# Kernel optimization log

Hardware: AMD Instinct MI355X
Metric: run time of the kernel (lower is better)

## Reference

```python
import jax, jax.numpy as jnp
import numpy as np

LMAX=4; MMAX=2; L2=25; M2=19; C=64; CE=64; NRBF=600; CUT=5.0
HEADS=8; ACH=32; VCH=16; HMSG=64; HFF=128; G=288; NL=2
AVG_NEI=20.0; AVG_NODES=2000.0
N_NODES=2000; N_EDGES=40000; NSPEC=90
# |m| group of each truncated (edge-frame) coefficient, order l=0..4, m=-min(l,2)..min(l,2)
MG = np.array([0, 1,0,1, 2,1,0,1,2, 2,1,0,1,2, 2,1,0,1,2])
# l of each full SH coefficient (25 total)
LOC = np.array([0] + [1]*3 + [2]*5 + [3]*7 + [4]*9)

def silu(x):
    return x * jax.nn.sigmoid(x)

def rms_norm_sh(x, w):
    # x: [N, 25, C]; w: [5, C] per-degree affine weight (rms_norm_sh)
    ms = jnp.mean(x * x, axis=1, keepdims=True)
    return x * jax.lax.rsqrt(ms + 1e-6) * w[LOC][None]

def setup_inputs() -> dict:
    key = jax.random.key(0)
    ks = iter(jax.random.split(key, 64))
    def rn(shape, scale):
        return jax.random.normal(next(ks), shape, dtype=jnp.float32) * scale
    inp = {}
    inp['edge_vectors'] = rn((N_EDGES, 3), 1.5)
    inp['wigner'] = rn((N_EDGES, M2, L2), 0.2)
    inp['wigner_inv'] = rn((N_EDGES, L2, M2), 0.2)
    inp['species_embed'] = rn((NSPEC, C), 1.0)
    inp['edge_species_embed'] = rn((NSPEC, 2 * CE), 1.0)
    DIN = NRBF + 2 * CE  # 728
    inp['deg_W1'] = rn((DIN, 128), DIN ** -0.5)
    inp['deg_b1'] = jnp.zeros((128,), jnp.float32)
    inp['deg_W2'] = rn((128, M2 * C), 128 ** -0.5)
    inp['deg_b2'] = jnp.zeros((M2 * C,), jnp.float32)
    inp['norm1_w'] = jnp.ones((NL, 5, C), jnp.float32)
    inp['rad_W1'] = rn((NL, DIN, 128), DIN ** -0.5)
    inp['rad_b1'] = jnp.zeros((NL, 128), jnp.float32)
    inp['rad_W2'] = rn((NL, 128, 3 * 2 * C), 128 ** -0.5)
    inp['rad_b2'] = jnp.ones((NL, 3 * 2 * C), jnp.float32)
    inp['so2_W'] = rn((NL, 3, 2 * C, HMSG), (2 * C) ** -0.5)
    inp['alpha_W'] = rn((NL, HMSG, HEADS * ACH), HMSG ** -0.5)
    inp['alpha_vec'] = rn((NL, HEADS, ACH), ACH ** -0.5)
    inp['value_W'] = rn((NL, 3, HMSG, HEADS * VCH), HMSG ** -0.5)
    inp['proj_W'] = rn((NL, 3, HEADS * VCH, C), (HEADS * VCH) ** -0.5)
    inp['norm2_w'] = jnp.ones((NL, 5, C), jnp.float32)
    inp['ffn_W1'] = rn((NL, C, HFF), C ** -0.5)
    inp['ffn_b1'] = jnp.zeros((NL, HFF), jnp.float32)
    inp['ffn_W2'] = rn((NL, HFF, C), HFF ** -0.5)
    inp['to_grid'] = rn((G, L2), L2 ** -0.5)
    inp['from_grid'] = rn((L2, G), G ** -0.5)
    inp['final_norm_w'] = jnp.ones((5, C), jnp.float32)
    inp['en_W1'] = rn((C, HFF), C ** -0.5)
    inp['en_b1'] = jnp.zeros((HFF,), jnp.float32)
    inp['en_W2'] = rn((HFF, 1), HFF ** -0.5)
    inp['en_b2'] = jnp.zeros((1,), jnp.float32)
    inp['node_species'] = jax.random.randint(next(ks), (N_NODES,), 0, NSPEC, dtype=jnp.int32)
    inp['senders'] = jax.random.randint(next(ks), (N_EDGES,), 0, N_NODES, dtype=jnp.int32)
    inp['receivers'] = jax.random.randint(next(ks), (N_EDGES,), 0, N_NODES, dtype=jnp.int32)
    inp['n_node'] = jnp.array([N_NODES], jnp.int32)
    return inp

def reference(edge_vectors, wigner, wigner_inv, species_embed, edge_species_embed,
              deg_W1, deg_b1, deg_W2, deg_b2, norm1_w, rad_W1, rad_b1, rad_W2, rad_b2,
              so2_W, alpha_W, alpha_vec, value_W, proj_W, norm2_w, ffn_W1, ffn_b1, ffn_W2,
              to_grid, from_grid, final_norm_w, en_W1, en_b1, en_W2, en_b2,
              node_species, senders, receivers, n_node):
    N = node_species.shape[0]
    E = senders.shape[0]
    mg = jnp.asarray(MG)
    # Gaussian RBF distance expansion (rbf_width=2.0)
    d = jnp.sqrt(jnp.sum(edge_vectors * edge_vectors, axis=-1) + 1e-12)
    offs = jnp.linspace(0.0, CUT, NRBF)
    std = 2.0 * (CUT / (NRBF - 1))
    rbf = jnp.exp(-0.5 * ((d[:, None] - offs[None, :]) / std) ** 2)  # [E, 600]
    # shared atom-edge embedding concat
    ne = edge_species_embed[node_species]
    se, re = jnp.split(ne, 2, axis=-1)
    ee = jnp.concatenate([rbf, se[senders], re[receivers]], axis=1)  # [E, 728]
    # initial node features: species embedding on l=0 component
    x = jnp.zeros((N, L2, C), dtype=edge_vectors.dtype).at[:, 0, :].set(species_embed[node_species])
    # edge degree embedding: radial MLP -> edge-frame coeffs -> rotate back -> scatter
    h = silu(ee @ deg_W1 + deg_b1) @ deg_W2 + deg_b2
    deg = jnp.einsum('elm,emc->elc', wigner_inv, h.reshape(E, M2, C))  # [E,25,C]
    x = x + jax.ops.segment_sum(deg, receivers, num_segments=N) / AVG_NEI
    for i in range(NL):
        # --- SO2 equivariant graph attention ---
        res = x
        xn = rms_norm_sh(x, norm1_w[i])
        msg = jnp.concatenate([xn[senders], xn[receivers]], axis=-1)      # [E,25,2C]
        msg = jnp.einsum('eml,elc->emc', wigner, msg)                     # rotate to edge frame [E,19,2C]
        rad = (silu(ee @ rad_W1[i] + rad_b1[i]) @ rad_W2[i] + rad_b2[i]).reshape(E, MMAX + 1, 2 * C)
        msg = msg * rad[:, mg]                                            # per-|m| radial modulation
        h = jnp.einsum('emc,mco->emo', msg, so2_W[i][mg])                 # SO2 conv [E,19,HMSG]
        a = (silu(h[:, 0, :]) @ alpha_W[i]).reshape(E, HEADS, ACH)        # invariant (m=0) alpha path
        logits = jnp.sum(silu(a) * alpha_vec[i][None], axis=-1)           # [E,HEADS]
        mx = jax.ops.segment_max(logits, receivers, num_segments=N)[receivers]
        ex = jnp.exp(logits - mx)
        den = jax.ops.segment_sum(ex, receivers, num_segments=N)[receivers]
        attn = ex / (den + 1e-12)
        v = jnp.einsum('emo,mov->emv', h, value_W[i][mg]).reshape(E, M2, HEADS, VCH)
        v = (v * attn[:, None, :, None]).reshape(E, M2, HEADS * VCH)
        oe = jnp.einsum('emv,mvc->emc', v, proj_W[i][mg])                 # [E,19,C]
        oe = jnp.einsum('elm,emc->elc', wigner_inv, oe)                   # rotate back [E,25,C]
        x = res + jax.ops.segment_sum(oe, receivers, num_segments=N)
        # --- S2 grid feed-forward ---
        res = x
        xn = rms_norm_sh(x, norm2_w[i])
        g = jnp.einsum('gl,nlc->ngc', to_grid, xn)                        # [N,288,C]
        g = silu(g @ ffn_W1[i] + ffn_b1[i]) @ ffn_W2[i]
        x = res + jnp.einsum('lg,ngc->nlc', from_grid, g)
    # final norm + energy head
    xn = rms_norm_sh(x, final_norm_w)
    g = jnp.einsum('gl,nlc->ngc', to_grid, xn)
    g = silu(g @ en_W1 + en_b1) @ en_W2 + en_b2
    eo = jnp.einsum('lg,ngo->nlo', from_grid, g)
    return eo[:, 0, 0] / AVG_NODES
```

## Files before the change

kernel.cpp:

```cpp
#include <hip/hip_runtime.h>
#include <hip/hip_bf16.h>
#include <math.h>


#define NRBF 600
#define DIN 728
#define GPTS 288
#define CH 8

typedef __attribute__((ext_vector_type(8))) short bf16x8;
typedef __attribute__((ext_vector_type(4))) float f32x4;

__constant__ int d_mg[19] = {0,1,0,1,2,1,0,1,2,2,1,0,1,2,2,1,0,1,2};
__constant__ int d_loc[25] = {0,1,1,1,2,2,2,2,2,3,3,3,3,3,3,3,4,4,4,4,4,4,4,4,4};
__constant__ int d_mg0[5]={0,2,6,11,16};
__constant__ int d_mg1[8]={1,3,5,7,10,12,15,17};
__constant__ int d_mg2[6]={4,8,9,13,14,18};

__device__ inline float silu_f(float v){ return v/(1.0f+__expf(-v)); }
__device__ inline float bf2f(unsigned short u){ return __uint_as_float(((unsigned)u)<<16); }
__device__ inline unsigned short f2bf(float f){
  unsigned b=__float_as_uint(f);
  return (unsigned short)((b + 0x7FFF + ((b>>16)&1)) >> 16);
}

__device__ inline void atomicMaxF(float* addr, float val){
  int* ia=(int*)addr;
  int old=*ia;
  while (__int_as_float(old) < val){
    int assumed=old;
    old = atomicCAS(ia, assumed, __float_as_int(val));
    if (old == assumed) break;
  }
}

__global__ __launch_bounds__(256) void zero_cnt_kernel(int* cnt, int N){
  int i = blockIdx.x*256+threadIdx.x;
  if (i<N) cnt[i]=0;
}
__global__ __launch_bounds__(256) void csr_count_kernel(const int* __restrict__ rcv, int* cnt, int E){
  int i = blockIdx.x*256+threadIdx.x;
  if (i<E) atomicAdd(&cnt[rcv[i]],1);
}
__global__ __launch_bounds__(256) void csr_scan_kernel(const int* __restrict__ cnt,
    int* rowptr, int* fill, int N){
  __shared__ int s_part[256];
  int tid=threadIdx.x;
  int chunk=(N+255)/256;
  int lvals[12];
  int base=tid*chunk;
  int lsum=0;
  for (int i=0;i<chunk && i<12;i++){
    int v=(base+i<N)?cnt[base+i]:0;
    lvals[i]=lsum; lsum+=v;
  }
  s_part[tid]=lsum;
  __syncthreads();
  if (tid==0){
    int run=0;
    for (int t=0;t<256;t++){ int v=s_part[t]; s_part[t]=run; run+=v; }
  }
  __syncthreads();
  int off=s_part[tid];
  for (int i=0;i<chunk && i<12;i++){
    if (base+i<N){ rowptr[base+i]=off+lvals[i]; fill[base+i]=off+lvals[i]; }
  }
  if (tid==255) rowptr[N]=off+lsum;
}
__global__ __launch_bounds__(256) void csr_fill_kernel(const int* __restrict__ rcv,
    int* fill, int* eix, int E){
  int i = blockIdx.x*256+threadIdx.x;
  if (i<E){ int p=atomicAdd(&fill[rcv[i]],1); eix[p]=i; }
}

__global__ __launch_bounds__(256) void wsvb_kernel(const float* __restrict__ so2W,
    const float* __restrict__ valW, unsigned short* __restrict__ wsvb){
  int i=blockIdx.x/3, g=blockIdx.x%3;
  const float* A = so2W + (size_t)i*24576 + g*8192;
  const float* B = valW + (size_t)i*24576 + g*8192;
  unsigned short* C = wsvb + (size_t)blockIdx.x*16384;
  __shared__ float sB[8192];
  for (int j=threadIdx.x;j<2048;j+=256) ((float4*)sB)[j]=((const float4*)B)[j];
  __syncthreads();
  for (int idx=threadIdx.x; idx<16384; idx+=256){
    int k=idx>>7, j=idx&127;
    float acc=0;
    #pragma unroll 4
    for (int o=0;o<64;o++) acc += A[k*64+o]*sB[o*128+j];
    int pos = ((k>>5)*8 + (j>>4))*512 + (((k>>3)&3)*16 + (j&15))*8 + (k&7);
    C[pos]=f2bf(acc);
  }
}

__global__ __launch_bounds__(256) void projb_kernel(const float* __restrict__ pW,
    unsigned short* __restrict__ projb){
  const float* src = pW + (size_t)blockIdx.x*8192;
  unsigned short* dst = projb + (size_t)blockIdx.x*8192;
  for (int idx=threadIdx.x; idx<8192; idx+=256){
    int k=idx>>6, j=idx&63;
    int pos = ((k>>5)*4 + (j>>4))*512 + (((k>>3)&3)*16 + (j&15))*8 + (k&7);
    dst[pos]=f2bf(src[idx]);
  }
}

__global__ __launch_bounds__(256) void packB2g_kernel(const float* __restrict__ src,
    unsigned short* __restrict__ dh, unsigned short* __restrict__ dl, int K, int Nn){
  int ktiles=(K+31)>>5;
  int nnt=Nn>>4;
  int tot=ktiles*nnt*512;
  for (int idx=blockIdx.x*256+threadIdx.x; idx<tot; idx+=gridDim.x*256){
    int f=idx>>9, r=idx&511, lane=r>>3, j=r&7;
    int kt=f/nnt, nt=f-kt*nnt;
    int k=kt*32+(lane>>4)*8+j, c=nt*16+(lane&15);
    float v=(k<K)? src[k*Nn+c] : 0.0f;
    unsigned short h=f2bf(v);
    dh[idx]=h;
    dl[idx]=f2bf(v-bf2f(h));
  }
}

__global__ __launch_bounds__(256) void pack_tg2_kernel(const float* __restrict__ tg,
    unsigned short* __restrict__ tgp){
  int tid=threadIdx.x;
  for (int idx=tid; idx<9216; idx+=256){
    int t=idx>>9, r=idx&511, lane=r>>3, j=r&7;
    int kl=(lane>>4)*8+j, row=t*16+(lane&15);
    float v=(kl<25)? tg[row*25+kl] : 0.0f;
    unsigned short h=f2bf(v);
    tgp[idx]=h;
    tgp[9216+idx]=f2bf(v-bf2f(h));
  }
}

__global__ __launch_bounds__(256) void pack_fg2_kernel(const float* __restrict__ fg,
    unsigned short* __restrict__ fgp){
  int tid=threadIdx.x;
  for (int idx=tid; idx<18432; idx+=256){
    int f=idx>>9, r=idx&511, lane=r>>3, j=r&7;
    int t=f>>1, mt=f&1;
    int row=mt*16+(lane&15), k=(lane>>4)*8+j;
    float v=(row<25 && k<16)? fg[row*288+t*16+k] : 0.0f;
    unsigned short h=f2bf(v);
    fgp[idx]=h;
    fgp[18432+idx]=f2bf(v-bf2f(h));
  }
}

__global__ __launch_bounds__(256) void mlpf_kernel(const float* __restrict__ ev,
    const float* __restrict__ ese, const int* __restrict__ nsp,
    const unsigned short* __restrict__ dw1h, const unsigned short* __restrict__ dw1l,
    const float* __restrict__ db1,
    const unsigned short* __restrict__ dw2h, const unsigned short* __restrict__ dw2l,
    const float* __restrict__ db2,
    const unsigned short* __restrict__ r1h, const unsigned short* __restrict__ r1l,
    const float* __restrict__ rb1,
    const unsigned short* __restrict__ r2h, const unsigned short* __restrict__ r2l,
    const float* __restrict__ rb2,
    const int* __restrict__ snd, const int* __restrict__ rcv, const int* __restrict__ eix,
    int do_deg,
    unsigned short* __restrict__ degout, float* __restrict__ radout, int E){
  int tid=threadIdx.x, wv=tid>>6, lane=tid&63;
  int lanelo=lane&15, khi=lane>>4;
  int p0=blockIdx.x*16;
  __shared__ unsigned short s_eeh[4096], s_eel[4096];
  __shared__ unsigned short s_h1h[2048], s_h1l[2048];
  __shared__ float s_d[16]; __shared__ int s_ss[16], s_rs[16], s_e[16];
  if (tid<16){
    int p=p0+tid;
    int e=(p<E)? eix[p] : -1;
    s_e[tid]=e;
    if (e>=0){
      float vx=ev[3*e], vy=ev[3*e+1], vz=ev[3*e+2];
      s_d[tid]=sqrtf(vx*vx+vy*vy+vz*vz+1e-12f);
      s_ss[tid]=nsp[snd[e]]; s_rs[tid]=nsp[rcv[e]];
    } else { s_d[tid]=0.0f; s_ss[tid]=0; s_rs[tid]=0; }
  }
  __syncthreads();
  const float step=5.0f/599.0f, inv_std=1.0f/(2.0f*step);
  int nta=wv*2, ntb=nta+1;
  f32x4 z4={0,0,0,0};
  f32x4 aD0=z4,aD1=z4,aR0=z4,aR1=z4;
  for (int c=0;c<23;c+=CH){
    int ncur=23-c; if (ncur>CH) ncur=CH;
    for (int idx=tid; idx<ncur*512; idx+=256){
      int f=idx>>9, r=idx&511, ln=r>>3, j=r&7;
      int k=(c+f)*32+((ln>>4)<<3)+j, row=ln&15;
      float v=0.0f;
      if (k<NRBF){ float t=(s_d[row]-k*step)*inv_std; v=__expf(-0.5f*t*t); }
      else if (k<NRBF+64) v=ese[s_ss[row]*128+(k-NRBF)];
      else if (k<DIN)     v=ese[s_rs[row]*128+64+(k-NRBF-64)];
      unsigned short h=f2bf(v);
      s_eeh[idx]=h; s_eel[idx]=f2bf(v-bf2f(h));
    }
    __syncthreads();
    for (int f=0; f<ncur; f++){
      int kt=c+f;
      bf16x8 Ah=*(const bf16x8*)(s_eeh + f*512 + lane*8);
      bf16x8 Al=*(const bf16x8*)(s_eel + f*512 + lane*8);
      size_t ba=(size_t)(kt*8+nta)*512+lane*8;
      {
        bf16x8 Bh=*(const bf16x8*)(r1h+ba), Bl=*(const bf16x8*)(r1l+ba);
        bf16x8 Bh2=*(const bf16x8*)(r1h+ba+512), Bl2=*(const bf16x8*)(r1l+ba+512);
        aR0=__builtin_amdgcn_mfma_f32_16x16x32_bf16(Ah,Bh,aR0,0,0,0);
        aR0=__builtin_amdgcn_mfma_f32_16x16x32_bf16(Al,Bh,aR0,0,0,0);
        aR0=__builtin_amdgcn_mfma_f32_16x16x32_bf16(Ah,Bl,aR0,0,0,0);
        aR1=__builtin_amdgcn_mfma_f32_16x16x32_bf16(Ah,Bh2,aR1,0,0,0);
        aR1=__builtin_amdgcn_mfma_f32_16x16x32_bf16(Al,Bh2,aR1,0,0,0);
        aR1=__builtin_amdgcn_mfma_f32_16x16x32_bf16(Ah,Bl2,aR1,0,0,0);
      }
      if (do_deg){
        bf16x8 Bh=*(const bf16x8*)(dw1h+ba), Bl=*(const bf16x8*)(dw1l+ba);
        bf16x8 Bh2=*(const bf16x8*)(dw1h+ba+512), Bl2=*(const bf16x8*)(dw1l+ba+512);
        aD0=__builtin_amdgcn_mfma_f32_16x16x32_bf16(Ah,Bh,aD0,0,0,0);
        aD0=__builtin_amdgcn_mfma_f32_16x16x32_bf16(Al,Bh,aD0,0,0,0);
        aD0=__builtin_amdgcn_mfma_f32_16x16x32_bf16(Ah,Bl,aD0,0,0,0);
        aD1=__builtin_amdgcn_mfma_f32_16x16x32_bf16(Ah,Bh2,aD1,0,0,0);
        aD1=__builtin_amdgcn_mfma_f32_16x16x32_bf16(Al,Bh2,aD1,0,0,0);
        aD1=__builtin_amdgcn_mfma_f32_16x16x32_bf16(Ah,Bl2,aD1,0,0,0);
      }
    }
    __syncthreads();
  }
  int nmlp = do_deg ? 2 : 1;
  #pragma unroll 1
  for (int it=0; it<nmlp; it++){
    int is_deg = (it==1);
    f32x4 a0 = is_deg ? aD0 : aR0;
    f32x4 a1 = is_deg ? aD1 : aR1;
    const float* b1 = is_deg ? db1 : rb1;
    #pragma unroll
    for (int q=0;q<4;q++){
      int row=khi*4+q;
      {
        int col=nta*16+lanelo;
        float v=silu_f(a0[q]+b1[col]);
        int pos=row*128 + (((col>>3)^(row&7))<<3) + (col&7);
        unsigned short h=f2bf(v);
        s_h1h[pos]=h; s_h1l[pos]=f2bf(v-bf2f(h));
      }
      {
        int col=ntb*16+lanelo;
        float v=silu_f(a1[q]+b1[col]);
        int pos=row*128 + (((col>>3)^(row&7))<<3) + (col&7);
        unsigned short h=f2bf(v);
        s_h1h[pos]=h; s_h1l[pos]=f2bf(v-bf2f(h));
      }
    }
    __syncthreads();
    bf16x8 Ahh[4],Ahl[4];
    #pragma unroll
    for (int kt=0;kt<4;kt++){
      int o=lanelo*128 + (((kt*4+khi)^(lanelo&7))<<3);
      Ahh[kt]=*(const bf16x8*)(s_h1h+o);
      Ahl[kt]=*(const bf16x8*)(s_h1l+o);
    }
    __syncthreads();
    if (is_deg){
      for (int nt=wv; nt<76; nt+=4){
        f32x4 acc=z4;
        #pragma unroll
        for (int kt=0;kt<4;kt++){
          size_t bo=(size_t)(kt*76+nt)*512+lane*8;
          bf16x8 Bh=*(const bf16x8*)(dw2h+bo), Bl=*(const bf16x8*)(dw2l+bo);
          acc=__builtin_amdgcn_mfma_f32_16x16x32_bf16(Ahh[kt],Bh,acc,0,0,0);
          acc=__builtin_amdgcn_mfma_f32_16x16x32_bf16(Ahl[kt],Bh,acc,0,0,0);
          acc=__builtin_amdgcn_mfma_f32_16x16x32_bf16(Ahh[kt],Bl,acc,0,0,0);
        }
        int col=nt*16+lanelo;
        float bb=db2[col];
        #pragma unroll
        for (int q=0;q<4;q++){
          int p=p0+khi*4+q;
          if (p<E) degout[(size_t)p*1216+col]=f2bf(acc[q]+bb);
        }
      }
    } else {
      for (int nt=wv; nt<24; nt+=4){
        f32x4 acc=z4;
        #pragma unroll
        for (int kt=0;kt<4;kt++){
          size_t bo=(size_t)(kt*24+nt)*512+lane*8;
          bf16x8 Bh=*(const bf16x8*)(r2h+bo), Bl=*(const bf16x8*)(r2l+bo);
          acc=__builtin_amdgcn_mfma_f32_16x16x32_bf16(Ahh[kt],Bh,acc,0,0,0);
          acc=__builtin_amdgcn_mfma_f32_16x16x32_bf16(Ahl[kt],Bh,acc,0,0,0);
          acc=__builtin_amdgcn_mfma_f32_16x16x32_bf16(Ahh[kt],Bl,acc,0,0,0);
        }
        int col=nt*16+lanelo;
        float bb=rb2[col];
        #pragma unroll
        for (int q=0;q<4;q++){
          int e=s_e[khi*4+q];
          if (e>=0) radout[(size_t)e*384+col]=acc[q]+bb;
        }
      }
    }
  }
}

__global__ __launch_bounds__(256) void node_sum_kernel(const unsigned short* __restrict__ msgb,
    const float* __restrict__ winv, const int* __restrict__ rowptr, const int* __restrict__ eix,
    const int* __restrict__ nsp, const float* __restrict__ spe,
    const float* __restrict__ nw, float* __restrict__ x, float* __restrict__ xn,
    int mode, int N){
  int n=blockIdx.x, tid=threadIdx.x, wv=tid>>6, lane=tid&63;
  __shared__ float s_winv[4][480];
  __shared__ unsigned short s_oe[4][1216];
  __shared__ float4 s_red[4][400];
  __shared__ float4 s_ms4[16];
  int row0=rowptr[n];
  int cnt=rowptr[n+1]-row0;
  float4 acc[7];
  #pragma unroll
  for (int t=0;t<7;t++) acc[t]=make_float4(0,0,0,0);
  for (int j=wv; j<cnt; j+=4){
    int p=row0+j;
    int e=eix[p];
    asm volatile("s_waitcnt lgkmcnt(0)" ::: "memory");
    for (int k=lane;k<475;k+=64) s_winv[wv][k]=winv[(size_t)e*475+k];
    if (mode==1){
      for (int k=lane;k<152;k+=64)
        ((int4*)s_oe[wv])[k]=*(const int4*)(msgb+(size_t)p*1216+k*8);
    } else {
      for (int k=lane;k<152;k+=64){
        int m=k>>3, jj=k&7;
        ((int4*)s_oe[wv])[k]=*(const int4*)(msgb+(size_t)p*2432+m*128+jj*8);
      }
    }
    asm volatile("s_waitcnt lgkmcnt(0)" ::: "memory");
    const unsigned* o2=(const unsigned*)s_oe[wv];
    #pragma unroll
    for (int t=0;t<7;t++){
      int sI=lane+t*64;
      if (sI<400){
        int l=sI>>4, c4=sI&15;
        const float* wr=s_winv[wv]+l*19;
        float4 a=acc[t];
        #pragma unroll
        for (int m=0;m<19;m++){
          float w=wr[m];
          unsigned ua=o2[m*32+c4*2], ub=o2[m*32+c4*2+1];
          a.x+=w*bf2f((unsigned short)(ua&0xffffu));
          a.y+=w*bf2f((unsigned short)(ua>>16));
          a.z+=w*bf2f((unsigned short)(ub&0xffffu));
          a.w+=w*bf2f((unsigned short)(ub>>16));
        }
        acc[t]=a;
      }
    }
  }
  asm volatile("s_waitcnt lgkmcnt(0)" ::: "memory");
  #pragma unroll
  for (int t=0;t<7;t++){
    int sI=lane+t*64;
    if (sI<400) s_red[wv][sI]=acc[t];
  }
  __syncthreads();
  float4* xp=(float4*)(x+(size_t)n*1600);
  int j0=tid, j1=tid+256;
  bool h1=(j1<400);
  float4 v0, v1=make_float4(0,0,0,0);
  if (mode==0){
    {
      float4 a=s_red[0][j0], b=s_red[1][j0], c=s_red[2][j0], d=s_red[3][j0];
      float4 cur=xp[j0];
      cur.x+=a.x+b.x+c.x+d.x;
      cur.y+=a.y+b.y+c.y+d.y;
      cur.z+=a.z+b.z+c.z+d.z;
      cur.w+=a.w+b.w+c.w+d.w;
      v0=cur; xp[j0]=cur;
    }
    if (h1){
      float4 a=s_red[0][j1], b=s_red[1][j1], c=s_red[2][j1], d=s_red[3][j1];
      float4 cur=xp[j1];
      cur.x+=a.x+b.x+c.x+d.x;
      cur.y+=a.y+b.y+c.y+d.y;
      cur.z+=a.z+b.z+c.z+d.z;
      cur.w+=a.w+b.w+c.w+d.w;
      v1=cur; xp[j1]=cur;
    }
  } else {
    int sp=nsp[n];
    const float4* sp4=(const float4*)(spe+(size_t)sp*64);
    {
      int l=j0>>4, c4=j0&15;
      float4 a=s_red[0][j0], b=s_red[1][j0], c=s_red[2][j0], d=s_red[3][j0];
      float4 base=(l==0)? sp4[c4] : make_float4(0,0,0,0);
      float4 o;
      o.x=base.x+0.05f*(a.x+b.x+c.x+d.x);
      o.y=base.y+0.05f*(a.y+b.y+c.y+d.y);
      o.z=base.z+0.05f*(a.z+b.z+c.z+d.z);
      o.w=base.w+0.05f*(a.w+b.w+c.w+d.w);
      v0=o; xp[j0]=o;
    }
    if (h1){
      float4 a=s_red[0][j1], b=s_red[1][j1], c=s_red[2][j1], d=s_red[3][j1];
      float4 o;
      o.x=0.05f*(a.x+b.x+c.x+d.x);
      o.y=0.05f*(a.y+b.y+c.y+d.y);
      o.z=0.05f*(a.z+b.z+c.z+d.z);
      o.w=0.05f*(a.w+b.w+c.w+d.w);
      v1=o; xp[j1]=o;
    }
  }
  __syncthreads();
  float4* s_p4=(float4*)s_red;
  float4 a4;
  a4.x=v0.x*v0.x; a4.y=v0.y*v0.y; a4.z=v0.z*v0.z; a4.w=v0.w*v0.w;
  if (h1){ a4.x+=v1.x*v1.x; a4.y+=v1.y*v1.y; a4.z+=v1.z*v1.z; a4.w+=v1.w*v1.w; }
  s_p4[tid]=a4;
  __syncthreads();
  if (tid<16){
    float4 s=make_float4(0,0,0,0);
    #pragma unroll
    for (int k=0;k<16;k++){
      float4 p=s_p4[tid+16*k];
      s.x+=p.x; s.y+=p.y; s.z+=p.z; s.w+=p.w;
    }
    float4 m;
    m.x=rsqrtf(s.x*(1.0f/25.0f)+1e-6f);
    m.y=rsqrtf(s.y*(1.0f/25.0f)+1e-6f);
    m.z=rsqrtf(s.z*(1.0f/25.0f)+1e-6f);
    m.w=rsqrtf(s.w*(1.0f/25.0f)+1e-6f);
    s_ms4[tid]=m;
  }
  __syncthreads();
  float4* xnp=(float4*)(xn+(size_t)n*1600);
  {
    int l=j0>>4, g=j0&15;
    float4 m=s_ms4[g];
    const float* wr=nw + d_loc[l]*64 + g*4;
    float4 o;
    o.x=v0.x*m.x*wr[0]; o.y=v0.y*m.y*wr[1]; o.z=v0.z*m.z*wr[2]; o.w=v0.w*m.w*wr[3];
    xnp[j0]=o;
  }
  if (h1){
    int l=j1>>4, g=j1&15;
    float4 m=s_ms4[g];
    const float* wr=nw + d_loc[l]*64 + g*4;
    float4 o;
    o.x=v1.x*m.x*wr[0]; o.y=v1.y*m.y*wr[1]; o.z=v1.z*m.z*wr[2]; o.w=v1.w*m.w*wr[3];
    xnp[j1]=o;
  }
}

__global__ __launch_bounds__(256) void init_mxden_kernel(float* mx, float* den, int N){
  int idx = blockIdx.x*256+threadIdx.x;
  if (idx < N*8){ mx[idx]=-3.0e38f; den[idx]=0.0f; }
}

__global__ __launch_bounds__(256) void den_kernel(const float* __restrict__ logits,
    const float* __restrict__ mx, const int* __restrict__ rcv,
    float* __restrict__ den, int E){
  int idx = blockIdx.x*256+threadIdx.x;
  if (idx >= E*8) return;
  int e = idx>>3, hd = idx&7, r = rcv[e];
  atomicAdd(&den[r*8+hd], __expf(logits[idx]-mx[r*8+hd]));
}

__global__ __launch_bounds__(256) void msg_kernel(const float* __restrict__ xn,
    const float* __restrict__ wig, const float* __restrict__ radb,
    const float* __restrict__ so2W, const float* __restrict__ alphaW, const float* __restrict__ alphaV,
    const int* __restrict__ snd, const int* __restrict__ rcv, const int* __restrict__ eix,
    unsigned short* __restrict__ msgb, float* __restrict__ logits, float* __restrict__ mx, int E){
  __shared__ float s_wig[1900];
  __shared__ float s_m0[4][128];
  __shared__ float s_sh0[4][64];
  int tid=threadIdx.x, wv=tid>>6, lane=tid&63;
  int p=blockIdx.x*4+wv;
  bool act=(p<E);
  int pc=act? p : (E-1);
  int e=eix[pc];
  int node=(lane<32)? snd[e] : rcv[e];
  int c2=(lane&31)*2;
  int col0=c2+((lane>>5)<<6);
  const float* xb=xn+(size_t)node*1600+c2;
  float ca[25], cb[25];
  #pragma unroll
  for (int l=0;l<25;l++){
    float2 v=*(const float2*)(xb+l*64);
    ca[l]=v.x; cb[l]=v.y;
  }
  float* swig=s_wig+wv*475;
  for (int j=lane;j<475;j+=64) swig[j]=wig[(size_t)e*475+j];
  float ra0,ra1,rb0,rb1,rc0,rc1;
  {
    const float* rb_=radb+(size_t)e*384;
    float2 v0=*(const float2*)(rb_+col0);
    float2 v1=*(const float2*)(rb_+128+col0);
    float2 v2=*(const float2*)(rb_+256+col0);
    ra0=v0.x; ra1=v0.y; rb0=v1.x; rb1=v1.y; rc0=v2.x; rc1=v2.y;
  }
  __syncthreads();
  unsigned short* dst=msgb+(size_t)pc*2432+col0;
  constexpr int mgc[19]={0,1,0,1,2,1,0,1,2,2,1,0,1,2,2,1,0,1,2};
  float m0a=0.0f, m0b=0.0f;
  if (act){
    #pragma unroll
    for (int m=0;m<19;m++){
      float a0=0.0f,a1=0.0f;
      const float* wr=swig+m*25;
      #pragma unroll
      for (int l=0;l<25;l++){ float w=wr[l]; a0+=w*ca[l]; a1+=w*cb[l]; }
      float r0,r1;
      if (mgc[m]==0){ r0=ra0; r1=ra1; }
      else if (mgc[m]==1){ r0=rb0; r1=rb1; }
      else { r0=rc0; r1=rc1; }
      a0*=r0; a1*=r1;
      if (m==0){ m0a=a0; m0b=a1; }
      unsigned packv=((unsigned)f2bf(a1)<<16)|(unsigned)f2bf(a0);
      *(unsigned*)(dst+m*128)=packv;
    }
  }
  s_m0[wv][col0]=m0a; s_m0[wv][col0+1]=m0b;
  asm volatile("s_waitcnt lgkmcnt(0)" ::: "memory");
  {
    const float* m0p=s_m0[wv];
    float accs=0.0f;
    #pragma unroll 8
    for (int k=0;k<128;k++) accs += m0p[k]*so2W[k*64+lane];
    s_sh0[wv][lane]=silu_f(accs);
  }
  asm volatile("s_waitcnt lgkmcnt(0)" ::: "memory");
  {
    const float* sh=s_sh0[wv];
    int j0=lane*4;
    float4 av=*(const float4*)(alphaV+j0);
    float4 aacc={0,0,0,0};
    #pragma unroll 8
    for (int o=0;o<64;o++){
      float s=sh[o];
      float4 w=*(const float4*)(alphaW+o*256+j0);
      aacc.x+=s*w.x; aacc.y+=s*w.y; aacc.z+=s*w.z; aacc.w+=s*w.w;
    }
    float part = silu_f(aacc.x)*av.x + silu_f(aacc.y)*av.y
               + silu_f(aacc.z)*av.z + silu_f(aacc.w)*av.w;
    part += __shfl_xor(part,1);
    part += __shfl_xor(part,2);
    part += __shfl_xor(part,4);
    if (act && (lane&7)==0){
      int h=lane>>3;
      int r=rcv[e];
      logits[(size_t)e*8+h]=part;
      atomicMaxF(&mx[r*8+h], part);
    }
  }
}

__global__ __launch_bounds__(256) void attn_gemm_kernel(unsigned short* __restrict__ msgb,
    const unsigned short* __restrict__ wsvp, const unsigned short* __restrict__ projp,
    const float* __restrict__ logits, const float* __restrict__ mx, const float* __restrict__ den,
    const int* __restrict__ eix, const int* __restrict__ rcv, int E){
  int tid=threadIdx.x, wv=tid>>6, lane=tid&63;
  int lanelo=lane&15, khi=lane>>4;
  int p0=blockIdx.x*16;
  __shared__ unsigned short s_vv[2176];
  __shared__ float s_attn[16][8];
  __shared__ short s_r2e[304], s_r2m[304];
  for (int j=tid;j<304;j+=256){
    int e,m;
    if (j<80){ e=j/5; m=d_mg0[j%5]; }
    else if (j<208){ int q=j-80; e=q>>3; m=d_mg1[q&7]; }
    else { int q=j-208; e=q/6; m=d_mg2[q%6]; }
    s_r2e[j]=(short)e; s_r2m[j]=(short)m;
  }
  if (tid<128){
    int i=tid>>3, h=tid&7, p=p0+i;
    float a=0.0f;
    if (p<E){
      int e=eix[p]; int r=rcv[e];
      a=__expf(logits[(size_t)e*8+h]-mx[r*8+h])/(den[r*8+h]+1e-12f);
    }
    s_attn[i][h]=a;
  }
  __syncthreads();
  const int4* wp4=(const int4*)wsvp;
  const int4* pp4=(const int4*)projp;
  for (int t=0;t<19;t++){
    int g=(t<5)?0:((t<13)?1:2);
    int R=t*16+lanelo;
    int ei=s_r2e[R], mi=s_r2m[R];
    int pp=p0+ei;
    size_t abase=((size_t)((pp<E)?pp:0))*2432 + (size_t)mi*128;
    bf16x8 A[4];
    #pragma unroll
    for (int kt=0;kt<4;kt++)
      A[kt]=*(const bf16x8*)(msgb + abase + kt*32 + khi*8);
    #pragma unroll
    for (int h2=0;h2<2;h2++){
      int nt=wv*2+h2;
      f32x4 acc={0,0,0,0};
      #pragma unroll
      for (int kt=0;kt<4;kt++){
        int4 tt=wp4[g*2048+(kt*8+nt)*64+lane];
        acc=__builtin_amdgcn_mfma_f32_16x16x32_bf16(A[kt],*(bf16x8*)&tt,acc,0,0,0);
      }
      int col=nt*16+lanelo;
      #pragma unroll
      for (int q=0;q<4;q++){
        int r16=khi*4+q;
        int ei2=s_r2e[t*16+r16];
        s_vv[r16*136+col]=f2bf(acc[q]*s_attn[ei2][nt]);
      }
    }
    __syncthreads();
    {
      bf16x8 A2[4];
      #pragma unroll
      for (int kt=0;kt<4;kt++)
        A2[kt]=*(const bf16x8*)(s_vv + lanelo*136 + kt*32 + khi*8);
      f32x4 acc={0,0,0,0};
      #pragma unroll
      for (int kt=0;kt<4;kt++){
        int4 tt=pp4[g*1024+(kt*4+wv)*64+lane];
        acc=__builtin_amdgcn_mfma_f32_16x16x32_bf16(A2[kt],*(bf16x8*)&tt,acc,0,0,0);
      }
      int col=wv*16+lanelo;
      #pragma unroll
      for (int q=0;q<4;q++){
        int R2=t*16+khi*4+q;
        int pi=p0+s_r2e[R2];
        if (pi<E) msgb[(size_t)pi*2432 + (size_t)s_r2m[R2]*128 + col]=f2bf(acc[q]);
      }
    }
    __syncthreads();
  }
}

__global__ __launch_bounds__(256) void grid_ffn_mfma_kernel(const float* __restrict__ xnin,
    const unsigned short* __restrict__ tgp, const unsigned short* __restrict__ fgp,
    const unsigned short* __restrict__ w1p, const unsigned short* __restrict__ w2p,
    const float* __restrict__ b1, const float* __restrict__ nw,
    float* __restrict__ x, float* __restrict__ xnout, int N){
  int n=blockIdx.x, tid=threadIdx.x, wv=tid>>6, lane=tid&63;
  int lanelo=lane&15, khi=lane>>4;
  __shared__ __align__(16) char s_mem[74240];
  unsigned short* s_w1=(unsigned short*)s_mem;
  unsigned short* s_xn=(unsigned short*)(s_mem+32768);
  float* s_b1=(float*)(s_mem+40960);
  unsigned short* scr=(unsigned short*)(s_mem+41472)+(size_t)wv*4096;
  for (int j=tid;j<2048;j+=256) ((int4*)s_w1)[j]=((const int4*)w1p)[j];
  if (tid<128) s_b1[tid]=b1[tid];
  { int4 z={0,0,0,0}; for (int j=tid;j<512;j+=256) ((int4*)s_xn)[j]=z; }
  __syncthreads();
  {
    const float* xr=xnin+(size_t)n*1600;
    for (int j=tid;j<1600;j+=256){
      int k=j>>6, c=j&63;
      float v=xr[j];
      unsigned short h=f2bf(v);
      s_xn[c*32+k]=h;
      s_xn[2048+c*32+k]=f2bf(v-bf2f(h));
    }
  }
  __syncthreads();
  bf16x8 XBh[4],XBl[4];
  #pragma unroll
  for (int ct=0;ct<4;ct++){
    int o=(ct*16+lanelo)*32 + khi*8;
    XBh[ct]=*(const bf16x8*)(s_xn+o);
    XBl[ct]=*(const bf16x8*)(s_xn+2048+o);
  }
  f32x4 oacc[2][4];
  #pragma unroll
  for (int mt=0;mt<2;mt++)
    #pragma unroll
    for (int nt=0;nt<4;nt++){ f32x4 z={0,0,0,0}; oacc[mt][nt]=z; }
  for (int t=wv;t<18;t+=4){
    bf16x8 Atgh=*(const bf16x8*)(tgp + t*512 + lane*8);
    bf16x8 Atgl=*(const bf16x8*)(tgp + 9216 + t*512 + lane*8);
    #pragma unroll
    for (int ct=0;ct<4;ct++){
      f32x4 g={0,0,0,0};
      g=__builtin_amdgcn_mfma_f32_16x16x32_bf16(Atgh,XBh[ct],g,0,0,0);
      g=__builtin_amdgcn_mfma_f32_16x16x32_bf16(Atgl,XBh[ct],g,0,0,0);
      g=__builtin_amdgcn_mfma_f32_16x16x32_bf16(Atgh,XBl[ct],g,0,0,0);
      #pragma unroll
      for (int q=0;q<4;q++){
        int row=khi*4+q, col=ct*16+lanelo;
        int pos=row*64 + (((col>>3)^(row&7))<<3) + (col&7);
        float v=g[q]; unsigned short h=f2bf(v);
        scr[pos]=h; scr[1024+pos]=f2bf(v-bf2f(h));
      }
    }
    bf16x8 Agh[2],Agl[2];
    #pragma unroll
    for (int kt=0;kt<2;kt++){
      int o=lanelo*64 + (((kt*4+khi)^(lanelo&7))<<3);
      Agh[kt]=*(const bf16x8*)(scr+o);
      Agl[kt]=*(const bf16x8*)(scr+1024+o);
    }
    #pragma unroll
    for (int nt=0;nt<8;nt++){
      f32x4 h={0,0,0,0};
      #pragma unroll
      for (int kt=0;kt<2;kt++){
        bf16x8 Bh=*(const bf16x8*)(s_w1 + (kt*8+nt)*512 + lane*8);
        bf16x8 Bl=*(const bf16x8*)(s_w1 + 8192 + (kt*8+nt)*512 + lane*8);
        h=__builtin_amdgcn_mfma_f32_16x16x32_bf16(Agh[kt],Bh,h,0,0,0);
        h=__builtin_amdgcn_mfma_f32_16x16x32_bf16(Agl[kt],Bh,h,0,0,0);
        h=__builtin_amdgcn_mfma_f32_16x16x32_bf16(Agh[kt],Bl,h,0,0,0);
      }
      #pragma unroll
      for (int q=0;q<4;q++){
        int row=khi*4+q, col=nt*16+lanelo;
        float v=silu_f(h[q]+s_b1[col]);
        int pos=row*128 + (((col>>3)^(row&7))<<3) + (col&7);
        unsigned short hh=f2bf(v);
        scr[pos]=hh; scr[2048+pos]=f2bf(v-bf2f(hh));
      }
    }
    bf16x8 Ahh[4],Ahl[4];
    #pragma unroll
    for (int kt=0;kt<4;kt++){
      int o=lanelo*128 + (((kt*4+khi)^(lanelo&7))<<3);
      Ahh[kt]=*(const bf16x8*)(scr+o);
      Ahl[kt]=*(const bf16x8*)(scr+2048+o);
    }
    #pragma unroll
    for (int nt=0;nt<4;nt++){
      f32x4 o4={0,0,0,0};
      #pragma unroll
      for (int kt=0;kt<4;kt++){
        bf16x8 Bh=*(const bf16x8*)(w2p + (kt*4+nt)*512 + lane*8);
        bf16x8 Bl=*(const bf16x8*)(w2p + 8192 + (kt*4+nt)*512 + lane*8);
        o4=__builtin_amdgcn_mfma_f32_16x16x32_bf16(Ahh[kt],Bh,o4,0,0,0);
        o4=__builtin_amdgcn_mfma_f32_16x16x32_bf16(Ahl[kt],Bh,o4,0,0,0);
        o4=__builtin_amdgcn_mfma_f32_16x16x32_bf16(Ahh[kt],Bl,o4,0,0,0);
      }
      #pragma unroll
      for (int q=0;q<4;q++){
        int ch=nt*16+lanelo, rowk=khi*4+q;
        int pos=ch*32 + (((rowk>>3)^(ch&3))<<3) + (rowk&7);
        float v=o4[q]; unsigned short hh=f2bf(v);
        scr[pos]=hh; scr[2048+pos]=f2bf(v-bf2f(hh));
      }
    }
    bf16x8 Boh[4],Bol[4];
    #pragma unroll
    for (int nt=0;nt<4;nt++){
      int ch=nt*16+lanelo;
      int o=ch*32 + ((khi^(ch&3))<<3);
      Boh[nt]=*(const bf16x8*)(scr+o);
      Bol[nt]=*(const bf16x8*)(scr+2048+o);
    }
    #pragma unroll
    for (int mt=0;mt<2;mt++){
      bf16x8 Afh=*(const bf16x8*)(fgp + (t*2+mt)*512 + lane*8);
      bf16x8 Afl=*(const bf16x8*)(fgp + 18432 + (t*2+mt)*512 + lane*8);
      #pragma unroll
      for (int nt=0;nt<4;nt++){
        oacc[mt][nt]=__builtin_amdgcn_mfma_f32_16x16x32_bf16(Afh,Boh[nt],oacc[mt][nt],0,0,0);
        oacc[mt][nt]=__builtin_amdgcn_mfma_f32_16x16x32_bf16(Afl,Boh[nt],oacc[mt][nt],0,0,0);
        oacc[mt][nt]=__builtin_amdgcn_mfma_f32_16x16x32_bf16(Afh,Bol[nt],oacc[mt][nt],0,0,0);
      }
    }
  }
  __syncthreads();
  float* pout=(float*)s_mem;
  #pragma unroll
  for (int mt=0;mt<2;mt++)
    #pragma unroll
    for (int nt=0;nt<4;nt++)
      #pragma unroll
      for (int q=0;q<4;q++){
        int row=mt*16+khi*4+q, col=nt*16+lanelo;
        pout[wv*2048 + row*64 + col]=oacc[mt][nt][q];
      }
  __syncthreads();
  const size_t nb=(size_t)n*1600;
  float accn=0.0f;
  for (int j=tid;j<1600;j+=256){
    float v = x[nb+j] + pout[j]+pout[2048+j]+pout[4096+j]+pout[6144+j];
    x[nb+j]=v;
    accn += v*v;
  }
  __syncthreads();
  float* s_part=(float*)s_mem;
  float* s_msv=((float*)s_mem)+256;
  s_part[tid]=accn;
  __syncthreads();
  if (tid<64){
    float m=(s_part[tid]+s_part[tid+64]+s_part[tid+128]+s_part[tid+192])*(1.0f/25.0f);
    s_msv[tid]=rsqrtf(m+1e-6f);
  }
  __syncthreads();
  for (int j=tid;j<1600;j+=256){
    int l=j>>6, c=j&63;
    xnout[nb+j]=x[nb+j]*s_msv[c]*nw[d_loc[l]*64+c];
  }
}

__global__ __launch_bounds__(256) void energy_mfma_kernel(const float* __restrict__ xn,
    const unsigned short* __restrict__ tgp, const float* __restrict__ fg,
    const unsigned short* __restrict__ enw1p, const float* __restrict__ b1,
    const float* __restrict__ w2, const float* __restrict__ b2,
    float* __restrict__ out, int N){
  int n=blockIdx.x, tid=threadIdx.x, wv=tid>>6, lane=tid&63;
  int lanelo=lane&15, khi=lane>>4;
  __shared__ __align__(16) char s_mem[59584];
  unsigned short* s_w1=(unsigned short*)s_mem;
  unsigned short* s_xn=(unsigned short*)(s_mem+32768);
  float* s_b1=(float*)(s_mem+40960);
  float* s_w2=(float*)(s_mem+41472);
  float* s_fg0=(float*)(s_mem+41984);
  float* s_red=(float*)(s_mem+43136);
  unsigned short* scr=(unsigned short*)(s_mem+43200)+(size_t)wv*2048;
  for (int j=tid;j<2048;j+=256) ((int4*)s_w1)[j]=((const int4*)enw1p)[j];
  if (tid<128){ s_b1[tid]=b1[tid]; s_w2[tid]=w2[tid]; }
  for (int j=tid;j<288;j+=256) s_fg0[j]=fg[j];
  { int4 z={0,0,0,0}; for (int j=tid;j<512;j+=256) ((int4*)s_xn)[j]=z; }
  __syncthreads();
  {
    const float* xr=xn+(size_t)n*1600;
    for (int j=tid;j<1600;j+=256){
      int k=j>>6, c=j&63;
      float v=xr[j];
      unsigned short h=f2bf(v);
      s_xn[c*32+k]=h;
      s_xn[2048+c*32+k]=f2bf(v-bf2f(h));
    }
  }
  __syncthreads();
  bf16x8 XBh[4],XBl[4];
  #pragma unroll
  for (int ct=0;ct<4;ct++){
    int o=(ct*16+lanelo)*32 + khi*8;
    XBh[ct]=*(const bf16x8*)(s_xn+o);
    XBl[ct]=*(const bf16x8*)(s_xn+2048+o);
  }
  float b2v=b2[0];
  float e=0.0f;
  for (int t=wv;t<18;t+=4){
    bf16x8 Atgh=*(const bf16x8*)(tgp + t*512 + lane*8);
    bf16x8 Atgl=*(const bf16x8*)(tgp + 9216 + t*512 + lane*8);
    #pragma unroll
    for (int ct=0;ct<4;ct++){
      f32x4 g={0,0,0,0};
      g=__builtin_amdgcn_mfma_f32_16x16x32_bf16(Atgh,XBh[ct],g,0,0,0);
      g=__builtin_amdgcn_mfma_f32_16x16x32_bf16(Atgl,XBh[ct],g,0,0,0);
      g=__builtin_amdgcn_mfma_f32_16x16x32_bf16(Atgh,XBl[ct],g,0,0,0);
      #pragma unroll
      for (int q=0;q<4;q++){
        int row=khi*4+q, col=ct*16+lanelo;
        int pos=row*64 + (((col>>3)^(row&7))<<3) + (col&7);
        float v=g[q]; unsigned short h=f2bf(v);
        scr[pos]=h; scr[1024+pos]=f2bf(v-bf2f(h));
      }
    }
    bf16x8 Agh[2],Agl[2];
    #pragma unroll
    for (int kt=0;kt<2;kt++){
      int o=lanelo*64 + (((kt*4+khi)^(lanelo&7))<<3);
      Agh[kt]=*(const bf16x8*)(scr+o);
      Agl[kt]=*(const bf16x8*)(scr+1024+o);
    }
    #pragma unroll
    for (int nt=0;nt<8;nt++){
      f32x4 h={0,0,0,0};
      #pragma unroll
      for (int kt=0;kt<2;kt++){
        bf16x8 Bh=*(const bf16x8*)(s_w1 + (kt*8+nt)*512 + lane*8);
        bf16x8 Bl=*(const bf16x8*)(s_w1 + 8192 + (kt*8+nt)*512 + lane*8);
        h=__builtin_amdgcn_mfma_f32_16x16x32_bf16(Agh[kt],Bh,h,0,0,0);
        h=__builtin_amdgcn_mfma_f32_16x16x32_bf16(Agl[kt],Bh,h,0,0,0);
        h=__builtin_amdgcn_mfma_f32_16x16x32_bf16(Agh[kt],Bl,h,0,0,0);
      }
      #pragma unroll
      for (int q=0;q<4;q++){
        int row=khi*4+q, col=nt*16+lanelo;
        float v=silu_f(h[q]+s_b1[col]);
        e += v*s_w2[col]*s_fg0[t*16+row];
      }
    }
    if (lanelo==0){
      #pragma unroll
      for (int q=0;q<4;q++) e += s_fg0[t*16+khi*4+q]*b2v;
    }
  }
  #pragma unroll
  for (int d=1;d<64;d<<=1) e += __shfl_xor(e,d);
  if (lane==0) s_red[wv]=e;
  __syncthreads();
  if (tid==0) out[n]=(s_red[0]+s_red[1]+s_red[2]+s_red[3])*(1.0f/2000.0f);
}

extern "C" void kernel_launch(void* const* d_in, const int* in_sizes, int n_in,
                              void* d_out, int out_size, void* d_ws, size_t ws_size,
                              hipStream_t stream){
  (void)n_in; (void)out_size; (void)ws_size;
  const float* ev   = (const float*)d_in[0];
  const float* wig  = (const float*)d_in[1];
  const float* winv = (const float*)d_in[2];
  const float* spe  = (const float*)d_in[3];
  const float* ese  = (const float*)d_in[4];
  const float* degW1= (const float*)d_in[5];
  const float* degb1= (const float*)d_in[6];
  const float* degW2= (const float*)d_in[7];
  const float* degb2= (const float*)d_in[8];
  const float* n1w  = (const float*)d_in[9];
  const float* radW1= (const float*)d_in[10];
  const float* radb1= (const float*)d_in[11];
  const float* radW2= (const float*)d_in[12];
  const float* radb2= (const float*)d_in[13];
  const float* so2W = (const float*)d_in[14];
  const float* aW   = (const float*)d_in[15];
  const float* aV   = (const float*)d_in[16];
  const float* vW   = (const float*)d_in[17];
  const float* pW   = (const float*)d_in[18];
  const float* n2w  = (const float*)d_in[19];
  const float* fW1  = (const float*)d_in[20];
  const float* fb1  = (const float*)d_in[21];
  const float* fW2  = (const float*)d_in[22];
  const float* tg   = (const float*)d_in[23];
  const float* fg   = (const float*)d_in[24];
  const float* fnw  = (const float*)d_in[25];
  const float* enW1 = (const float*)d_in[26];
  const float* enb1 = (const float*)d_in[27];
  const float* enW2 = (const float*)d_in[28];
  const float* enb2 = (const float*)d_in[29];
  const int* nsp = (const int*)d_in[30];
  const int* snd = (const int*)d_in[31];
  const int* rcv = (const int*)d_in[32];
  int N = in_sizes[30];
  int E = in_sizes[31];
  float* out = (float*)d_out;

  float* ws = (float*)d_ws;
  size_t off = 0;
  float* radbuf = ws + off; off += (size_t)E*384;
  float* logits = ws + off; off += (size_t)E*8;
  float* mx     = ws + off; off += (size_t)N*8;
  float* den    = ws + off; off += (size_t)N*8;
  float* x      = ws + off; off += (size_t)N*1600;
  float* xn     = ws + off; off += (size_t)N*1600;
  unsigned short* wsvb  = (unsigned short*)(ws + off); off += (size_t)6*16384/2;
  unsigned short* projb = (unsigned short*)(ws + off); off += (size_t)6*8192/2;
  int* cnt      = (int*)(ws + off); off += (size_t)N;
  int* rowptr   = (int*)(ws + off); off += (size_t)(N+1);
  int* fill     = (int*)(ws + off); off += (size_t)N;
  int* eixbuf   = (int*)(ws + off); off += (size_t)E;
  off = (off + 3) & ~((size_t)3);
  unsigned short* msgb  = (unsigned short*)(ws + off); off += (size_t)E*1216;
  unsigned short* tgp   = (unsigned short*)(ws + off); off += 9216;
  unsigned short* fgp   = (unsigned short*)(ws + off); off += 18432;
  unsigned short* wwp   = (unsigned short*)(ws + off); off += 32768;
  unsigned short* enw1p = (unsigned short*)(ws + off); off += 8192;
  unsigned short* degw1p = (unsigned short*)(ws + off); off += 94208;
  unsigned short* degw2p = (unsigned short*)(ws + off); off += 155648;
  unsigned short* radw1p = (unsigned short*)(ws + off); off += 94208*2;
  unsigned short* radw2p = (unsigned short*)(ws + off); off += 49152*2;

  zero_cnt_kernel<<<(N+255)/256, 256, 0, stream>>>(cnt, N);
  csr_count_kernel<<<(E+255)/256, 256, 0, stream>>>(rcv, cnt, E);
  csr_scan_kernel<<<1, 256, 0, stream>>>(cnt, rowptr, fill, N);
  csr_fill_kernel<<<(E+255)/256, 256, 0, stream>>>(rcv, fill, eixbuf, E);
  wsvb_kernel<<<6, 256, 0, stream>>>(so2W, vW, wsvb);
  projb_kernel<<<6, 256, 0, stream>>>(pW, projb);
  pack_tg2_kernel<<<1, 256, 0, stream>>>(tg, tgp);
  pack_fg2_kernel<<<1, 256, 0, stream>>>(fg, fgp);
  for (int i=0;i<2;i++){
    unsigned short* wl = wwp + (size_t)i*32768;
    packB2g_kernel<<<8, 256, 0, stream>>>(fW1 + (size_t)i*8192, wl, wl+8192, 64, 128);
    packB2g_kernel<<<8, 256, 0, stream>>>(fW2 + (size_t)i*8192, wl+16384, wl+24576, 128, 64);
  }
  packB2g_kernel<<<8, 256, 0, stream>>>(enW1, enw1p, enw1p+8192, 64, 128);
  packB2g_kernel<<<32, 256, 0, stream>>>(degW1, degw1p, degw1p+94208, DIN, 128);
  packB2g_kernel<<<32, 256, 0, stream>>>(degW2, degw2p, degw2p+155648, 128, 1216);
  for (int i=0;i<2;i++){
    unsigned short* r1 = radw1p + (size_t)i*188416;
    unsigned short* r2 = radw2p + (size_t)i*98304;
    packB2g_kernel<<<32, 256, 0, stream>>>(radW1 + (size_t)i*DIN*128, r1, r1+94208, DIN, 128);
    packB2g_kernel<<<16, 256, 0, stream>>>(radW2 + (size_t)i*128*384, r2, r2+49152, 128, 384);
  }

  mlpf_kernel<<<(E+15)/16, 256, 0, stream>>>(ev, ese, nsp,
      degw1p, degw1p+94208, degb1, degw2p, degw2p+155648, degb2,
      radw1p, radw1p+94208, radb1,
      radw2p, radw2p+49152, radb2,
      snd, rcv, eixbuf, 1, msgb, radbuf, E);
  node_sum_kernel<<<N, 256, 0, stream>>>(msgb, winv, rowptr, eixbuf, nsp, spe,
                                         n1w, x, xn, 1, N);

  for (int i=0;i<2;i++){
    if (i==1){
      unsigned short* r1 = radw1p + (size_t)188416;
      unsigned short* r2 = radw2p + (size_t)98304;
      mlpf_kernel<<<(E+15)/16, 256, 0, stream>>>(ev, ese, nsp,
          degw1p, degw1p+94208, degb1, degw2p, degw2p+155648, degb2,
          r1, r1+94208, radb1+128,
          r2, r2+49152, radb2+384,
          snd, rcv, eixbuf, 0, msgb, radbuf, E);
    }
    init_mxden_kernel<<<(N*8+255)/256, 256, 0, stream>>>(mx, den, N);
    msg_kernel<<<(E+3)/4, 256, 0, stream>>>(xn, wig, radbuf,
                                            so2W + (size_t)i*24576,
                                            aW + (size_t)i*64*256, aV + (size_t)i*256,
                                            snd, rcv, eixbuf, msgb, logits, mx, E);
    den_kernel<<<(E*8+255)/256, 256, 0, stream>>>(logits, mx, rcv, den, E);
    attn_gemm_kernel<<<(E+15)/16, 256, 0, stream>>>(msgb,
                                                    wsvb + (size_t)i*3*16384, projb + (size_t)i*3*8192,
                                                    logits, mx, den, eixbuf, rcv, E);
    node_sum_kernel<<<N, 256, 0, stream>>>(msgb, winv, rowptr, eixbuf, nsp, spe,
                                           n2w + (size_t)i*320, x, xn, 0, N);
    const float* nxt = (i==0) ? (n1w + 320) : fnw;
    grid_ffn_mfma_kernel<<<N, 256, 0, stream>>>(xn, tgp, fgp,
                                                wwp + (size_t)i*32768, wwp + (size_t)i*32768 + 16384,
                                                fb1 + (size_t)i*128, nxt, x, xn, N);
  }
  energy_mfma_kernel<<<N, 256, 0, stream>>>(xn, tgp, fg, enw1p, enb1, enW2, enb2, out, N);
}
```

Measured before the change: 2.731 ms.

## Fuse both layers' radial MLPs into the single edge-feature MLP kernel

The second mlpf launch for layer 1 is removed. The first launch now computes the radial MLP hidden layers for both layers, alongside the degree MLP, from the same RBF and species feature tiles, so those features are built once. Radial outputs are stored as bf16 in two separate buffers instead of fp32, which halves the radial write and read traffic in msg_kernel. The cost is higher register pressure in the fused kernel and lower precision for the radial weights.

Result: slower. 2.806 ms (+2.8%).

```diff
diff --git a/kernel.cpp b/kernel.cpp
--- a/kernel.cpp
+++ b/kernel.cpp
@@ -152,13 +152,17 @@
     const float* __restrict__ db1,
     const unsigned short* __restrict__ dw2h, const unsigned short* __restrict__ dw2l,
     const float* __restrict__ db2,
-    const unsigned short* __restrict__ r1h, const unsigned short* __restrict__ r1l,
-    const float* __restrict__ rb1,
-    const unsigned short* __restrict__ r2h, const unsigned short* __restrict__ r2l,
-    const float* __restrict__ rb2,
+    const unsigned short* __restrict__ r1h0, const unsigned short* __restrict__ r1l0,
+    const float* __restrict__ rb10,
+    const unsigned short* __restrict__ r2h0, const unsigned short* __restrict__ r2l0,
+    const float* __restrict__ rb20,
+    const unsigned short* __restrict__ r1h1, const unsigned short* __restrict__ r1l1,
+    const float* __restrict__ rb11,
+    const unsigned short* __restrict__ r2h1, const unsigned short* __restrict__ r2l1,
+    const float* __restrict__ rb21,
     const int* __restrict__ snd, const int* __restrict__ rcv, const int* __restrict__ eix,
-    int do_deg,
-    unsigned short* __restrict__ degout, float* __restrict__ radout, int E){
+    unsigned short* __restrict__ degout,
+    unsigned short* __restrict__ rad0out, unsigned short* __restrict__ rad1out, int E){
   int tid=threadIdx.x, wv=tid>>6, lane=tid&63;
   int lanelo=lane&15, khi=lane>>4;
   int p0=blockIdx.x*16;
@@ -179,7 +183,7 @@
   const float step=5.0f/599.0f, inv_std=1.0f/(2.0f*step);
   int nta=wv*2, ntb=nta+1;
   f32x4 z4={0,0,0,0};
-  f32x4 aD0=z4,aD1=z4,aR0=z4,aR1=z4;
+  f32x4 aD0=z4,aD1=z4,aR0=z4,aR1=z4,aS0=z4,aS1=z4;
   for (int c=0;c<23;c+=CH){
     int ncur=23-c; if (ncur>CH) ncur=CH;
     for (int idx=tid; idx<ncur*512; idx+=256){
@@ -199,8 +203,8 @@
       bf16x8 Al=*(const bf16x8*)(s_eel + f*512 + lane*8);
       size_t ba=(size_t)(kt*8+nta)*512+lane*8;
       {
-        bf16x8 Bh=*(const bf16x8*)(r1h+ba), Bl=*(const bf16x8*)(r1l+ba);
-        bf16x8 Bh2=*(const bf16x8*)(r1h+ba+512), Bl2=*(const bf16x8*)(r1l+ba+512);
+        bf16x8 Bh=*(const bf16x8*)(r1h0+ba), Bl=*(const bf16x8*)(r1l0+ba);
+        bf16x8 Bh2=*(const bf16x8*)(r1h0+ba+512), Bl2=*(const bf16x8*)(r1l0+ba+512);
         aR0=__builtin_amdgcn_mfma_f32_16x16x32_bf16(Ah,Bh,aR0,0,0,0);
         aR0=__builtin_amdgcn_mfma_f32_16x16x32_bf16(Al,Bh,aR0,0,0,0);
         aR0=__builtin_amdgcn_mfma_f32_16x16x32_bf16(Ah,Bl,aR0,0,0,0);
@@ -208,7 +212,17 @@
         aR1=__builtin_amdgcn_mfma_f32_16x16x32_bf16(Al,Bh2,aR1,0,0,0);
         aR1=__builtin_amdgcn_mfma_f32_16x16x32_bf16(Ah,Bl2,aR1,0,0,0);
       }
-      if (do_deg){
+      {
+        bf16x8 Bh=*(const bf16x8*)(r1h1+ba), Bl=*(const bf16x8*)(r1l1+ba);
+        bf16x8 Bh2=*(const bf16x8*)(r1h1+ba+512), Bl2=*(const bf16x8*)(r1l1+ba+512);
+        aS0=__builtin_amdgcn_mfma_f32_16x16x32_bf16(Ah,Bh,aS0,0,0,0);
+        aS0=__builtin_amdgcn_mfma_f32_16x16x32_bf16(Al,Bh,aS0,0,0,0);
+        aS0=__builtin_amdgcn_mfma_f32_16x16x32_bf16(Ah,Bl,aS0,0,0,0);
+        aS1=__builtin_amdgcn_mfma_f32_16x16x32_bf16(Ah,Bh2,aS1,0,0,0);
+        aS1=__builtin_amdgcn_mfma_f32_16x16x32_bf16(Al,Bh2,aS1,0,0,0);
+        aS1=__builtin_amdgcn_mfma_f32_16x16x32_bf16(Ah,Bl2,aS1,0,0,0);
+      }
+      {
         bf16x8 Bh=*(const bf16x8*)(dw1h+ba), Bl=*(const bf16x8*)(dw1l+ba);
         bf16x8 Bh2=*(const bf16x8*)(dw1h+ba+512), Bl2=*(const bf16x8*)(dw1l+ba+512);
         aD0=__builtin_amdgcn_mfma_f32_16x16x32_bf16(Ah,Bh,aD0,0,0,0);
@@ -221,13 +235,11 @@
     }
     __syncthreads();
   }
-  int nmlp = do_deg ? 2 : 1;
   #pragma unroll 1
-  for (int it=0; it<nmlp; it++){
-    int is_deg = (it==1);
-    f32x4 a0 = is_deg ? aD0 : aR0;
-    f32x4 a1 = is_deg ? aD1 : aR1;
-    const float* b1 = is_deg ? db1 : rb1;
+  for (int it=0; it<3; it++){
+    f32x4 a0 = (it==0)? aR0 : (it==1)? aS0 : aD0;
+    f32x4 a1 = (it==0)? aR1 : (it==1)? aS1 : aD1;
+    const float* b1 = (it==0)? rb10 : (it==1)? rb11 : db1;
     #pragma unroll
     for (int q=0;q<4;q++){
       int row=khi*4+q;
@@ -255,7 +267,7 @@
       Ahl[kt]=*(const bf16x8*)(s_h1l+o);
     }
     __syncthreads();
-    if (is_deg){
+    if (it==2){
       for (int nt=wv; nt<76; nt+=4){
         f32x4 acc=z4;
         #pragma unroll
@@ -275,22 +287,26 @@
         }
       }
     } else {
+      const unsigned short* w2h = (it==0)? r2h0 : r2h1;
+      const unsigned short* w2l = (it==0)? r2l0 : r2l1;
+      const float* b2p = (it==0)? rb20 : rb21;
+      unsigned short* ro = (it==0)? rad0out : rad1out;
       for (int nt=wv; nt<24; nt+=4){
         f32x4 acc=z4;
         #pragma unroll
         for (int kt=0;kt<4;kt++){
           size_t bo=(size_t)(kt*24+nt)*512+lane*8;
-          bf16x8 Bh=*(const bf16x8*)(r2h+bo), Bl=*(const bf16x8*)(r2l+bo);
+          bf16x8 Bh=*(const bf16x8*)(w2h+bo), Bl=*(const bf16x8*)(w2l+bo);
           acc=__builtin_amdgcn_mfma_f32_16x16x32_bf16(Ahh[kt],Bh,acc,0,0,0);
           acc=__builtin_amdgcn_mfma_f32_16x16x32_bf16(Ahl[kt],Bh,acc,0,0,0);
           acc=__builtin_amdgcn_mfma_f32_16x16x32_bf16(Ahh[kt],Bl,acc,0,0,0);
         }
         int col=nt*16+lanelo;
-        float bb=rb2[col];
+        float bb=b2p[col];
         #pragma unroll
         for (int q=0;q<4;q++){
           int e=s_e[khi*4+q];
-          if (e>=0) radout[(size_t)e*384+col]=acc[q]+bb;
+          if (e>=0) ro[(size_t)e*384+col]=f2bf(acc[q]+bb);
         }
       }
     }
@@ -458,7 +474,7 @@
 }
 
 __global__ __launch_bounds__(256) void msg_kernel(const float* __restrict__ xn,
-    const float* __restrict__ wig, const float* __restrict__ radb,
+    const float* __restrict__ wig, const unsigned short* __restrict__ radb,
     const float* __restrict__ so2W, const float* __restrict__ alphaW, const float* __restrict__ alphaV,
     const int* __restrict__ snd, const int* __restrict__ rcv, const int* __restrict__ eix,
     unsigned short* __restrict__ msgb, float* __restrict__ logits, float* __restrict__ mx, int E){
@@ -484,11 +500,13 @@
   for (int j=lane;j<475;j+=64) swig[j]=wig[(size_t)e*475+j];
   float ra0,ra1,rb0,rb1,rc0,rc1;
   {
-    const float* rb_=radb+(size_t)e*384;
-    float2 v0=*(const float2*)(rb_+col0);
-    float2 v1=*(const float2*)(rb_+128+col0);
-    float2 v2=*(const float2*)(rb_+256+col0);
-    ra0=v0.x; ra1=v0.y; rb0=v1.x; rb1=v1.y; rc0=v2.x; rc1=v2.y;
+    const unsigned short* rb_=radb+(size_t)e*384;
+    unsigned u0=*(const unsigned*)(rb_+col0);
+    unsigned u1=*(const unsigned*)(rb_+128+col0);
+    unsigned u2=*(const unsigned*)(rb_+256+col0);
+    ra0=bf2f((unsigned short)(u0&0xffffu)); ra1=bf2f((unsigned short)(u0>>16));
+    rb0=bf2f((unsigned short)(u1&0xffffu)); rb1=bf2f((unsigned short)(u1>>16));
+    rc0=bf2f((unsigned short)(u2&0xffffu)); rc1=bf2f((unsigned short)(u2>>16));
   }
   __syncthreads();
   unsigned short* dst=msgb+(size_t)pc*2432+col0;
@@ -927,7 +945,8 @@
 
   float* ws = (float*)d_ws;
   size_t off = 0;
-  float* radbuf = ws + off; off += (size_t)E*384;
+  unsigned short* rad0b = (unsigned short*)(ws + off); off += (size_t)E*192;
+  unsigned short* rad1b = (unsigned short*)(ws + off); off += (size_t)E*192;
   float* logits = ws + off; off += (size_t)E*8;
   float* mx     = ws + off; off += (size_t)N*8;
   float* den    = ws + off; off += (size_t)N*8;
@@ -977,22 +996,16 @@
       degw1p, degw1p+94208, degb1, degw2p, degw2p+155648, degb2,
       radw1p, radw1p+94208, radb1,
       radw2p, radw2p+49152, radb2,
-      snd, rcv, eixbuf, 1, msgb, radbuf, E);
+      radw1p+188416, radw1p+188416+94208, radb1+128,
+      radw2p+98304, radw2p+98304+49152, radb2+384,
+      snd, rcv, eixbuf, msgb, rad0b, rad1b, E);
   node_sum_kernel<<<N, 256, 0, stream>>>(msgb, winv, rowptr, eixbuf, nsp, spe,
                                          n1w, x, xn, 1, N);
 
   for (int i=0;i<2;i++){
-    if (i==1){
-      unsigned short* r1 = radw1p + (size_t)188416;
-      unsigned short* r2 = radw2p + (size_t)98304;
-      mlpf_kernel<<<(E+15)/16, 256, 0, stream>>>(ev, ese, nsp,
-          degw1p, degw1p+94208, degb1, degw2p, degw2p+155648, degb2,
-          r1, r1+94208, radb1+128,
-          r2, r2+49152, radb2+384,
-          snd, rcv, eixbuf, 0, msgb, radbuf, E);
-    }
     init_mxden_kernel<<<(N*8+255)/256, 256, 0, stream>>>(mx, den, N);
-    msg_kernel<<<(E+3)/4, 256, 0, stream>>>(xn, wig, radbuf,
+    const unsigned short* radp = (i==0)? rad0b : rad1b;
+    msg_kernel<<<(E+3)/4, 256, 0, stream>>>(xn, wig, radp,
                                             so2W + (size_t)i*24576,
                                             aW + (size_t)i*64*256, aV + (size_t)i*256,
                                             snd, rcv, eixbuf, msgb, logits, mx, E);
```
